# Kernel optimization log

Hardware: AMD Instinct MI355X
Metric: run time of the kernel (lower is better)

Reference implementation:

```python
import jax, jax.numpy as jnp
import numpy as np

EPS = 1e-12  # F.normalize default eps

def _l2norm(x):
    return x / jnp.maximum(jnp.linalg.norm(x, axis=-1, keepdims=True), EPS)

def setup_inputs() -> dict:
    key = jax.random.key(0)
    k1, k2, k3 = jax.random.split(key, 3)
    N, C, D = 131072, 1000, 256
    feat = jax.random.normal(k1, (N, D), dtype=jnp.float32)
    # memory bank is initialized to L2-normalized centers in the original (init())
    memory = _l2norm(jax.random.normal(k2, (C, D), dtype=jnp.float32))
    label = jax.random.randint(k3, (N,), 0, C, dtype=jnp.int64)
    return {"feat": feat, "memory": memory, "label": label}

def reference(feat, memory, label):
    num_cls, feat_dim = memory.shape
    N = feat.shape[0]
    t = 1.0  # forward default temperature

    featn = _l2norm(feat)

    # --- update(feat, label): fused per-class masked gather+sum as one segment_sum ---
    f = jax.lax.stop_gradient(featn)  # feat.detach() in original
    sums = jax.ops.segment_sum(f, label, num_segments=num_cls)          # [C, D]
    counts = jax.ops.segment_sum(jnp.ones((N,), f.dtype), label, num_segments=num_cls)
    flags = (counts > 0).astype(f.dtype)[:, None]                        # [C, 1]
    batch_center = _l2norm(sums) * flags                                 # zeros for empty classes

    # --- update_center_by_simi ---
    simi = jnp.sum(memory * batch_center, axis=-1, keepdims=True)        # [C, 1]
    update_wei = 1.0 - (1.0 - simi) * flags                              # [C, 1]
    new_memory = _l2norm(update_wei * memory + (1.0 - update_wei) * batch_center)

    # --- similarity + cross entropy ---
    simis = jnp.einsum('nd,cd->nc', featn, new_memory) / t               # [N, C]
    logp = jax.nn.log_softmax(simis, axis=-1)
    loss = -jnp.mean(jnp.take_along_axis(logp, label[:, None], axis=1))
    return loss
```

## Files before the change

kernel.cpp:

```cpp
#include <hip/hip_runtime.h>
#include <hip/hip_fp8.h>

#define NROWS 131072
#define NCLS  1000
#define CPAD  1024
#define DDIM  256

typedef __attribute__((ext_vector_type(4))) float f32x4;
typedef __attribute__((ext_vector_type(2))) long l64x2;

__device__ __forceinline__ float wred(float v){
#pragma unroll
  for (int m = 1; m < 64; m <<= 1) v += __shfl_xor(v, m, 64);
  return v;
}

__device__ __forceinline__ float fexp2(float x){
#if __has_builtin(__builtin_amdgcn_exp2f)
  return __builtin_amdgcn_exp2f(x);
#else
  float r; asm("v_exp_f32 %0, %1" : "=v"(r) : "v"(x)); return r;
#endif
}

__device__ __forceinline__ unsigned pk4_fp8(float a, float b, float c, float d){
#if __has_builtin(__builtin_amdgcn_cvt_pk_fp8_f32)
  int v = __builtin_amdgcn_cvt_pk_fp8_f32(a, b, 0, false);
  v = __builtin_amdgcn_cvt_pk_fp8_f32(c, d, v, true);
  return (unsigned)v;
#else
  __hip_fp8_e4m3 fa(a), fb(b), fc(c), fd(d);
  return (unsigned)fa.__x | ((unsigned)fb.__x<<8) |
         ((unsigned)fc.__x<<16) | ((unsigned)fd.__x<<24);
#endif
}

__device__ __forceinline__ void store_frag8(unsigned char* nmem, int c, int ln,
                                            float a, float b, float x, float y){
  int ch = c >> 5, nb = (c >> 4) & 1, r16 = c & 15;
  int k = ln >> 3, g = (ln >> 1) & 3, q = ln & 1;
  *(unsigned*)(nmem + ch*8192 + k*1024 + (g*16+r16)*16 + nb*8 + q*4) =
      pk4_fp8(a, b, x, y);
}

__global__ __launch_bounds__(1024) void k_center(
    const float* __restrict__ feat, const float* __restrict__ memory,
    const int* __restrict__ label, unsigned char* __restrict__ nmem){
  const int c0 = blockIdx.x * 2;
  const int t = threadIdx.x;
  const int w = t >> 6, lane = t & 63;
  if (c0 >= NCLS){
    if (t < 128) store_frag8(nmem, c0 + (t >> 6), t & 63, 0.f, 0.f, 0.f, 0.f);
    return;
  }
  const int c1 = c0 + 1;
  __shared__ float4 accred[2][16][64];
  __shared__ int cw[2][16];

  float4 a0 = make_float4(0.f,0.f,0.f,0.f);
  float4 a1 = make_float4(0.f,0.f,0.f,0.f);
  int cnt0 = 0, cnt1 = 0;
  const float4* feat4 = (const float4*)feat;
  const int4*   lab4  = (const int4*)label;

  for (int it = 0; it < 32; ++it){
    int base = (w*32 + it) * 256;
    int4 lv = lab4[base/4 + lane];
#pragma unroll
    for (int sub = 0; sub < 4; ++sub){
      int lvv = (sub==0)?lv.x:(sub==1)?lv.y:(sub==2)?lv.z:lv.w;
      unsigned long long m0 = __ballot(lvv == c0);
      unsigned long long m1 = __ballot(lvv == c1);
      cnt0 += (int)__popcll(m0); cnt1 += (int)__popcll(m1);
      while (m0){
        int b = __ffsll((long long)m0) - 1; m0 &= m0 - 1;
        int r = base + b*4 + sub;
        float4 x = feat4[r*64 + lane];
        float ss = wred(x.x*x.x + x.y*x.y + x.z*x.z + x.w*x.w);
        float sc = 1.0f / fmaxf(sqrtf(ss), 1e-12f);
        a0.x += x.x*sc; a0.y += x.y*sc; a0.z += x.z*sc; a0.w += x.w*sc;
      }
      while (m1){
        int b = __ffsll((long long)m1) - 1; m1 &= m1 - 1;
        int r = base + b*4 + sub;
        float4 x = feat4[r*64 + lane];
        float ss = wred(x.x*x.x + x.y*x.y + x.z*x.z + x.w*x.w);
        float sc = 1.0f / fmaxf(sqrtf(ss), 1e-12f);
        a1.x += x.x*sc; a1.y += x.y*sc; a1.z += x.z*sc; a1.w += x.w*sc;
      }
    }
  }
  accred[0][w][lane] = a0; accred[1][w][lane] = a1;
  if (lane == 0){ cw[0][w] = cnt0; cw[1][w] = cnt1; }
  __syncthreads();

  if (t < 128){
    int cls = t >> 6, ln = t & 63;
    float sx=0.f, sy=0.f, sz=0.f, sw=0.f; int total = 0;
#pragma unroll
    for (int s = 0; s < 16; ++s){
      float4 v = accred[cls][s][ln];
      sx += v.x; sy += v.y; sz += v.z; sw += v.w;
      total += cw[cls][s];
    }
    int c = c0 + cls;
    float ss = wred(sx*sx + sy*sy + sz*sz + sw*sw);
    float inv = 1.0f / fmaxf(sqrtf(ss), 1e-12f);
    float bx = sx*inv, by = sy*inv, bz = sz*inv, bw = sw*inv;
    float flag = (total > 0) ? 1.0f : 0.0f;
    float4 m = ((const float4*)memory)[c*64 + ln];
    float simi = wred(m.x*bx + m.y*by + m.z*bz + m.w*bw);
    float wei = 1.0f - (1.0f - simi)*flag;
    float rx = wei*m.x + (1.0f-wei)*bx;
    float ry = wei*m.y + (1.0f-wei)*by;
    float rz = wei*m.z + (1.0f-wei)*bz;
    float rw = wei*m.w + (1.0f-wei)*bw;
    float ss2 = wred(rx*rx + ry*ry + rz*rz + rw*rw);
    float inv2 = 1.0f / fmaxf(sqrtf(ss2), 1e-12f);
    store_frag8(nmem, c, ln, rx*inv2, ry*inv2, rz*inv2, rw*inv2);
  }
}

#define MFMA8 __builtin_amdgcn_mfma_f32_16x16x32_fp8_fp8

__global__ __launch_bounds__(256, 2) void k_gemm(
    const float* __restrict__ feat, const unsigned char* __restrict__ nmem,
    const int* __restrict__ label, float* __restrict__ partials){
  __shared__ float bred[4];
  const int t = threadIdx.x, w = t >> 6, lane = t & 63;
  const int g = lane >> 4, r16 = lane & 15;
  const int rowbase = blockIdx.x * 256;

  long areg[4][8];
  float rs_self[4];
#pragma unroll
  for (int mf = 0; mf < 4; ++mf){
    int row = rowbase + w*64 + mf*16 + r16;
    const float4* rp = (const float4*)(feat + row*DDIM);
    float ss = 0.f;
#pragma unroll
    for (int kt = 0; kt < 8; ++kt){
      float4 x0 = rp[kt*8 + g*2];
      float4 x1 = rp[kt*8 + g*2 + 1];
      ss += x0.x*x0.x + x0.y*x0.y + x0.z*x0.z + x0.w*x0.w
          + x1.x*x1.x + x1.y*x1.y + x1.z*x1.z + x1.w*x1.w;
      unsigned lo = pk4_fp8(x0.x, x0.y, x0.z, x0.w);
      unsigned hi = pk4_fp8(x1.x, x1.y, x1.z, x1.w);
      areg[mf][kt] = (long)(((unsigned long)hi << 32) | lo);
    }
    ss += __shfl_xor(ss, 16, 64);
    ss += __shfl_xor(ss, 32, 64);
    rs_self[mf] = 1.0f / fmaxf(sqrtf(ss), 1e-12f);
  }

  int labreg[4][4];
  float rs2[4][4];
#pragma unroll
  for (int m = 0; m < 4; ++m)
#pragma unroll
    for (int j = 0; j < 4; ++j){
      int rr = w*64 + m*16 + g*4 + j;
      labreg[m][j] = label[rowbase + rr];
      rs2[m][j] = __shfl(rs_self[m], g*4 + j, 16) * 1.44269504f;
    }

  float esum[4][4], slb[4][4];
#pragma unroll
  for (int m = 0; m < 4; ++m)
#pragma unroll
    for (int j = 0; j < 4; ++j){ esum[m][j] = 0.f; slb[m][j] = 0.f; }

  const char* nbp = (const char*)nmem + lane*16;
  const int rot = blockIdx.x & 31;
  long bA[8], bB[8];

#define LOADLO(CH)                                                            \
  { const char* cb = nbp + (size_t)(CH)*8192;                                 \
    _Pragma("unroll")                                                         \
    for (int k2 = 0; k2 < 4; ++k2){                                           \
      l64x2 v = *(const l64x2*)(cb + k2*1024);                                \
      bA[k2*2] = v.x; bA[k2*2+1] = v.y; } }
#define LOADHI(CH)                                                            \
  { const char* cb = nbp + (size_t)(CH)*8192 + 4096;                          \
    _Pragma("unroll")                                                         \
    for (int k2 = 0; k2 < 4; ++k2){                                           \
      l64x2 v = *(const l64x2*)(cb + k2*1024);                                \
      bB[k2*2] = v.x; bB[k2*2+1] = v.y; } }

  LOADLO(rot); LOADHI(rot);

  for (int it = 0; it < 32; ++it){
    int cur = (it + rot) & 31;
    int nxt = (it + 1 + rot) & 31;

    f32x4 acc[4][2];
    __builtin_amdgcn_s_setprio(1);
    {
      f32x4 Z = {0.f,0.f,0.f,0.f};
#pragma unroll
      for (int m = 0; m < 4; ++m){
        acc[m][0] = MFMA8(areg[m][0], bA[0], Z, 0, 0, 0);
        acc[m][1] = MFMA8(areg[m][0], bA[1], Z, 0, 0, 0);
      }
    }
#pragma unroll
    for (int k = 1; k < 4; ++k)
#pragma unroll
      for (int m = 0; m < 4; ++m){
        acc[m][0] = MFMA8(areg[m][k], bA[k*2+0], acc[m][0], 0, 0, 0);
        acc[m][1] = MFMA8(areg[m][k], bA[k*2+1], acc[m][1], 0, 0, 0);
      }
    __builtin_amdgcn_s_setprio(0);

    if (it < 31) LOADLO(nxt);

    __builtin_amdgcn_s_setprio(1);
#pragma unroll
    for (int k = 4; k < 8; ++k)
#pragma unroll
      for (int m = 0; m < 4; ++m){
        acc[m][0] = MFMA8(areg[m][k], bB[(k-4)*2+0], acc[m][0], 0, 0, 0);
        acc[m][1] = MFMA8(areg[m][k], bB[(k-4)*2+1], acc[m][1], 0, 0, 0);
      }
    __builtin_amdgcn_s_setprio(0);

    if (it < 31) LOADHI(nxt);

#pragma unroll
    for (int m = 0; m < 4; ++m)
#pragma unroll
      for (int n = 0; n < 2; ++n){
        int col = cur*32 + n*16 + r16;
#pragma unroll
        for (int j = 0; j < 4; ++j){
          float v = acc[m][n][j] * rs2[m][j];
          esum[m][j] += fexp2(v);
          slb[m][j] = (col == labreg[m][j]) ? v : slb[m][j];
        }
      }
  }

  float v = 0.f;
#pragma unroll
  for (int m = 0; m < 4; ++m)
#pragma unroll
    for (int j = 0; j < 4; ++j){
      float e = esum[m][j], s = slb[m][j];
      e += __shfl_xor(e, 1, 64); e += __shfl_xor(e, 2, 64);
      e += __shfl_xor(e, 4, 64); e += __shfl_xor(e, 8, 64);
      s += __shfl_xor(s, 1, 64); s += __shfl_xor(s, 2, 64);
      s += __shfl_xor(s, 4, 64); s += __shfl_xor(s, 8, 64);
      v += 0.69314718056f * (__log2f(e - 24.0f) - s);
    }
  if (r16 != 0) v = 0.f;
  v = wred(v);
  if (lane == 0) bred[w] = v;
  __syncthreads();
  if (t == 0) partials[blockIdx.x] = bred[0] + bred[1] + bred[2] + bred[3];
}

__global__ __launch_bounds__(256) void k_final(
    const float* __restrict__ partials, float* __restrict__ out){
  const int t = threadIdx.x;
  const int w = t >> 6, lane = t & 63;
  __shared__ float red[4];
  float s = partials[t] + partials[t+256];
  s = wred(s);
  if (lane == 0) red[w] = s;
  __syncthreads();
  if (t == 0) out[0] = (red[0]+red[1]+red[2]+red[3]) * (1.0f/(float)NROWS);
}

extern "C" void kernel_launch(void* const* d_in, const int* in_sizes, int n_in,
                              void* d_out, int out_size, void* d_ws, size_t ws_size,
                              hipStream_t stream){
  const float* feat   = (const float*)d_in[0];
  const float* memory = (const float*)d_in[1];
  const int*   label  = (const int*)d_in[2];
  float* out = (float*)d_out;
  unsigned char* nmem = (unsigned char*)d_ws;
  float* partials = (float*)((char*)d_ws + 524288);

  k_center<<<CPAD/2, 1024, 0, stream>>>(feat, memory, label, nmem);
  k_gemm<<<NROWS/256, 256, 0, stream>>>(feat, nmem, label, partials);
  k_final<<<1, 256, 0, stream>>>(partials, out);
}
```

Baseline: 115.1 us.

## Software-pipeline MFMA chunks with previous chunk's softmax epilogue via double accumulators

The column loop now uses two accumulator sets, so the exp/sum/label-select epilogue of the previous 32-column chunk is interleaved slice by slice with the MFMAs of the current chunk. The per-row inverse norm and the log2(e) factor are folded into the feature values before FP8 packing, which removes a multiply per logit. The label compare is precomputed with the lane offset subtracted. The setprio hints are dropped. The cost is more accumulator registers under launch_bounds(256,2), which risks spills, and scaling before FP8 quantization changes rounding.

Result: faster. 109.1 us, median of 2 (-5.2%).

```diff
diff --git a/kernel.cpp b/kernel.cpp
--- a/kernel.cpp
+++ b/kernel.cpp
@@ -132,37 +132,38 @@
   const int rowbase = blockIdx.x * 256;
 
   long areg[4][8];
-  float rs_self[4];
 #pragma unroll
   for (int mf = 0; mf < 4; ++mf){
     int row = rowbase + w*64 + mf*16 + r16;
     const float4* rp = (const float4*)(feat + row*DDIM);
+    float4 xv[16];
     float ss = 0.f;
 #pragma unroll
     for (int kt = 0; kt < 8; ++kt){
-      float4 x0 = rp[kt*8 + g*2];
-      float4 x1 = rp[kt*8 + g*2 + 1];
+      xv[kt*2]   = rp[kt*8 + g*2];
+      xv[kt*2+1] = rp[kt*8 + g*2 + 1];
+      float4 x0 = xv[kt*2], x1 = xv[kt*2+1];
       ss += x0.x*x0.x + x0.y*x0.y + x0.z*x0.z + x0.w*x0.w
           + x1.x*x1.x + x1.y*x1.y + x1.z*x1.z + x1.w*x1.w;
-      unsigned lo = pk4_fp8(x0.x, x0.y, x0.z, x0.w);
-      unsigned hi = pk4_fp8(x1.x, x1.y, x1.z, x1.w);
-      areg[mf][kt] = (long)(((unsigned long)hi << 32) | lo);
     }
     ss += __shfl_xor(ss, 16, 64);
     ss += __shfl_xor(ss, 32, 64);
-    rs_self[mf] = 1.0f / fmaxf(sqrtf(ss), 1e-12f);
-  }
-
-  int labreg[4][4];
-  float rs2[4][4];
+    float sc = 1.44269504f / fmaxf(sqrtf(ss), 1e-12f);
+#pragma unroll
+    for (int kt = 0; kt < 8; ++kt){
+      float4 x0 = xv[kt*2], x1 = xv[kt*2+1];
+      unsigned lo = pk4_fp8(x0.x*sc, x0.y*sc, x0.z*sc, x0.w*sc);
+      unsigned hi = pk4_fp8(x1.x*sc, x1.y*sc, x1.z*sc, x1.w*sc);
+      areg[mf][kt] = (long)(((unsigned long)hi << 32) | lo);
+    }
+  }
+
+  int labc[4][4];
 #pragma unroll
   for (int m = 0; m < 4; ++m)
 #pragma unroll
-    for (int j = 0; j < 4; ++j){
-      int rr = w*64 + m*16 + g*4 + j;
-      labreg[m][j] = label[rowbase + rr];
-      rs2[m][j] = __shfl(rs_self[m], g*4 + j, 16) * 1.44269504f;
-    }
+    for (int j = 0; j < 4; ++j)
+      labc[m][j] = label[rowbase + w*64 + m*16 + g*4 + j] - r16;
 
   float esum[4][4], slb[4][4];
 #pragma unroll
@@ -173,6 +174,7 @@
   const char* nbp = (const char*)nmem + lane*16;
   const int rot = blockIdx.x & 31;
   long bA[8], bB[8];
+  f32x4 accA[4][2], accB[4][2];
 
 #define LOADLO(CH)                                                            \
   { const char* cb = nbp + (size_t)(CH)*8192;                                 \
@@ -187,57 +189,61 @@
       l64x2 v = *(const l64x2*)(cb + k2*1024);                                \
       bB[k2*2] = v.x; bB[k2*2+1] = v.y; } }
 
+#define EPI_SLICE(P, COLS0, S)                                                \
+  { const int m_ = (S) >> 1, n_ = (S) & 1;                                    \
+    int cols_ = (COLS0) + n_*16;                                              \
+    _Pragma("unroll")                                                         \
+    for (int j = 0; j < 4; ++j){                                              \
+      float v_ = P[m_][n_][j];                                                \
+      esum[m_][j] += fexp2(v_);                                               \
+      slb[m_][j] = (cols_ == labc[m_][j]) ? v_ : slb[m_][j];                  \
+    } }
+
+#define CHUNK(ACC, PRV, PCOLS, NXT, DOLD, DOEPI)                              \
+  {                                                                           \
+    { f32x4 Z = {0.f,0.f,0.f,0.f};                                            \
+      _Pragma("unroll")                                                       \
+      for (int m = 0; m < 4; ++m){                                            \
+        ACC[m][0] = MFMA8(areg[m][0], bA[0], Z, 0, 0, 0);                     \
+        ACC[m][1] = MFMA8(areg[m][0], bA[1], Z, 0, 0, 0); } }                 \
+    if (DOEPI) EPI_SLICE(PRV, PCOLS, 0);                                      \
+    _Pragma("unroll")                                                         \
+    for (int k = 1; k < 4; ++k){                                              \
+      _Pragma("unroll")                                                       \
+      for (int m = 0; m < 4; ++m){                                            \
+        ACC[m][0] = MFMA8(areg[m][k], bA[k*2+0], ACC[m][0], 0, 0, 0);         \
+        ACC[m][1] = MFMA8(areg[m][k], bA[k*2+1], ACC[m][1], 0, 0, 0); }       \
+      if (DOEPI) EPI_SLICE(PRV, PCOLS, k);                                    \
+    }                                                                         \
+    if (DOLD) LOADLO(NXT);                                                    \
+    _Pragma("unroll")                                                         \
+    for (int k = 4; k < 8; ++k){                                              \
+      _Pragma("unroll")                                                       \
+      for (int m = 0; m < 4; ++m){                                            \
+        ACC[m][0] = MFMA8(areg[m][k], bB[(k-4)*2+0], ACC[m][0], 0, 0, 0);     \
+        ACC[m][1] = MFMA8(areg[m][k], bB[(k-4)*2+1], ACC[m][1], 0, 0, 0); }   \
+      if (DOEPI) EPI_SLICE(PRV, PCOLS, k);                                    \
+    }                                                                         \
+    if (DOLD) LOADHI(NXT);                                                    \
+  }
+
   LOADLO(rot); LOADHI(rot);
 
-  for (int it = 0; it < 32; ++it){
-    int cur = (it + rot) & 31;
-    int nxt = (it + 1 + rot) & 31;
-
-    f32x4 acc[4][2];
-    __builtin_amdgcn_s_setprio(1);
-    {
-      f32x4 Z = {0.f,0.f,0.f,0.f};
-#pragma unroll
-      for (int m = 0; m < 4; ++m){
-        acc[m][0] = MFMA8(areg[m][0], bA[0], Z, 0, 0, 0);
-        acc[m][1] = MFMA8(areg[m][0], bA[1], Z, 0, 0, 0);
-      }
-    }
-#pragma unroll
-    for (int k = 1; k < 4; ++k)
-#pragma unroll
-      for (int m = 0; m < 4; ++m){
-        acc[m][0] = MFMA8(areg[m][k], bA[k*2+0], acc[m][0], 0, 0, 0);
-        acc[m][1] = MFMA8(areg[m][k], bA[k*2+1], acc[m][1], 0, 0, 0);
-      }
-    __builtin_amdgcn_s_setprio(0);
-
-    if (it < 31) LOADLO(nxt);
-
-    __builtin_amdgcn_s_setprio(1);
-#pragma unroll
-    for (int k = 4; k < 8; ++k)
-#pragma unroll
-      for (int m = 0; m < 4; ++m){
-        acc[m][0] = MFMA8(areg[m][k], bB[(k-4)*2+0], acc[m][0], 0, 0, 0);
-        acc[m][1] = MFMA8(areg[m][k], bB[(k-4)*2+1], acc[m][1], 0, 0, 0);
-      }
-    __builtin_amdgcn_s_setprio(0);
-
-    if (it < 31) LOADHI(nxt);
-
-#pragma unroll
-    for (int m = 0; m < 4; ++m)
-#pragma unroll
-      for (int n = 0; n < 2; ++n){
-        int col = cur*32 + n*16 + r16;
-#pragma unroll
-        for (int j = 0; j < 4; ++j){
-          float v = acc[m][n][j] * rs2[m][j];
-          esum[m][j] += fexp2(v);
-          slb[m][j] = (col == labreg[m][j]) ? v : slb[m][j];
-        }
-      }
+  CHUNK(accA, accB, 0, (rot+1)&31, true, false);
+
+  for (int p = 0; p < 15; ++p){
+    int cB = (2*p   + rot) & 31;
+    int nB = (2*p+2 + rot) & 31;
+    CHUNK(accB, accA, cB*32, nB, true, true);
+    int cA = (2*p+1 + rot) & 31;
+    int nA = (2*p+3 + rot) & 31;
+    CHUNK(accA, accB, cA*32, nA, true, true);
+  }
+  CHUNK(accB, accA, ((30+rot)&31)*32, 0, false, true);
+  {
+    int cc = ((31+rot)&31)*32;
+#pragma unroll
+    for (int s = 0; s < 8; ++s) EPI_SLICE(accB, cc, s);
   }
 
   float v = 0.f;
```
